# Performance work log

Hardware: AMD Instinct MI355X
Metric: run time of the kernel (lower is better)

The kernel has to match this reference:

```python
import jax, jax.numpy as jnp
import numpy as np

B, L, H, W, C = 8, 512, 768, 12, 25
S = L * W          # span_idx count, reshaped to [B, L, W, H]
Hh = H // 2        # per-direction LSTM hidden (bidirectional)


def setup_inputs() -> dict:
    key = jax.random.key(0)
    ks = jax.random.split(key, 24)
    p = lambda k, shape: jax.random.normal(k, shape, jnp.float32) * 0.02
    z = lambda n: jnp.zeros((n,), jnp.float32)
    return {
        "we": jax.random.normal(ks[0], (B, L, H), jnp.float32),
        "mask": jnp.ones((B, L), jnp.int32),
        "span_idx": jax.random.randint(ks[1], (B, S, 2), 0, L, jnp.int32),
        "pe": jax.random.normal(ks[2], (B, C, H), jnp.float32),
        # BiLSTM params (PyTorch gate order i,f,g,o)
        "w_ih_f": p(ks[3], (4 * Hh, H)), "w_hh_f": p(ks[4], (4 * Hh, Hh)),
        "b_ih_f": z(4 * Hh), "b_hh_f": z(4 * Hh),
        "w_ih_b": p(ks[5], (4 * Hh, H)), "w_hh_b": p(ks[6], (4 * Hh, Hh)),
        "b_ih_b": z(4 * Hh), "b_hh_b": z(4 * Hh),
        # project_start MLP: H -> 4H -> H
        "start_w1": p(ks[7], (4 * H, H)), "start_b1": z(4 * H),
        "start_w2": p(ks[8], (H, 4 * H)), "start_b2": z(H),
        # project_end MLP
        "end_w1": p(ks[9], (4 * H, H)), "end_b1": z(4 * H),
        "end_w2": p(ks[10], (H, 4 * H)), "end_b2": z(H),
        # out_project MLP: 2H -> 4H -> H
        "out_w1": p(ks[11], (4 * H, 2 * H)), "out_b1": z(4 * H),
        "out_w2": p(ks[12], (H, 4 * H)), "out_b2": z(H),
        # prompt_proj MLP: H -> 4H -> H
        "pr_w1": p(ks[13], (4 * H, H)), "pr_b1": z(4 * H),
        "pr_w2": p(ks[14], (H, 4 * H)), "pr_b2": z(H),
    }


def lstm_dir(x, w_ih, w_hh, b_ih, b_hh, reverse):
    # x: [B,L,D] -> per-direction hidden sequence [B,L,Hh]
    xg = jnp.einsum('bld,gd->blg', x, w_ih) + b_ih  # precomputed input gates
    n = w_hh.shape[1]

    def step(carry, xg_t):
        h, c = carry
        g = xg_t + h @ w_hh.T + b_hh
        i, f, gg, o = jnp.split(g, 4, axis=-1)
        c = jax.nn.sigmoid(f) * c + jax.nn.sigmoid(i) * jnp.tanh(gg)
        h = jax.nn.sigmoid(o) * jnp.tanh(c)
        return (h, c), h

    init = (jnp.zeros((x.shape[0], n), x.dtype), jnp.zeros((x.shape[0], n), x.dtype))
    _, hs = jax.lax.scan(step, init, jnp.swapaxes(xg, 0, 1), reverse=reverse)
    return jnp.swapaxes(hs, 0, 1)


def mlp(x, w1, b1, w2, b2):
    # Linear -> ReLU -> (Dropout: identity in eval) -> Linear
    return jax.nn.relu(x @ w1.T + b1) @ w2.T + b2


def extract_elements(t, idx):
    # t: [B,L,D], idx: [B,S] -> [B,S,D]; indices clamped like torch
    idx = jnp.clip(idx, 0, t.shape[1] - 1)
    return jnp.take_along_axis(t, idx[..., None], axis=1)


def reference(we, mask, span_idx, pe,
              w_ih_f, w_hh_f, b_ih_f, b_hh_f,
              w_ih_b, w_hh_b, b_ih_b, b_hh_b,
              start_w1, start_b1, start_w2, start_b2,
              end_w1, end_b1, end_w2, end_b2,
              out_w1, out_b1, out_w2, out_b2,
              pr_w1, pr_b1, pr_w2, pr_b2):
    # 1) Bidirectional LSTM encoder (pad_packed zeros masked positions)
    hf = lstm_dir(we, w_ih_f, w_hh_f, b_ih_f, b_hh_f, reverse=False)
    hb = lstm_dir(we, w_ih_b, w_hh_b, b_ih_b, b_hh_b, reverse=True)
    h = jnp.concatenate([hf, hb], axis=-1) * mask[..., None].astype(we.dtype)
    # 2) SpanMarkerV0: dual MLP -> gather -> concat+relu -> out MLP
    start_rep = mlp(h, start_w1, start_b1, start_w2, start_b2)
    end_rep = mlp(h, end_w1, end_b1, end_w2, end_b2)
    ss = extract_elements(start_rep, span_idx[:, :, 0])
    es = extract_elements(end_rep, span_idx[:, :, 1])
    cat = jax.nn.relu(jnp.concatenate([ss, es], axis=-1))
    span = mlp(cat, out_w1, out_b1, out_w2, out_b2).reshape(B, L, W, H)
    # 3) Prompt projection
    prompt = mlp(pe, pr_w1, pr_b1, pr_w2, pr_b2)
    return (span, prompt)
```

## Files before the change

### kernel.cpp

```cpp
#include <hip/hip_runtime.h>
#include <hip/hip_bf16.h>
#include <stdint.h>

#define B_ 8
#define L_ 512
#define H_ 768
#define WW_ 12
#define C_ 25
#define S_ (L_*WW_)
#define HH 384
#define G4 1536

using bf16x8 = __attribute__((ext_vector_type(8))) short;
using f32x4  = __attribute__((ext_vector_type(4))) float;

static __device__ __forceinline__ unsigned short f2bf(float x){
  unsigned u = __float_as_uint(x);
  unsigned r = (u + 0x7FFFu + ((u >> 16) & 1u)) >> 16;
  return (unsigned short)r;
}
static __device__ __forceinline__ float bflo(unsigned u){ return __uint_as_float(u << 16); }
static __device__ __forceinline__ float bfhi(unsigned u){ return __uint_as_float(u & 0xFFFF0000u); }

static __device__ __forceinline__ float sigmoid_f(float x){
  x = fminf(15.f, fmaxf(-15.f, x));
  return 1.f / (1.f + __expf(-x));
}
static __device__ __forceinline__ float tanh_f(float x){
  x = fminf(15.f, fmaxf(-15.f, x));
  float e = __expf(-2.f * x);
  return (1.f - e) / (1.f + e);
}

static __device__ __forceinline__ void gl_lds16(const unsigned short* g, unsigned short* l){
  __builtin_amdgcn_global_load_lds(
      (const __attribute__((address_space(1))) unsigned int*)g,
      (__attribute__((address_space(3))) unsigned int*)l,
      16, 0, 0);
}

__global__ void k_cast_bf16(const float* __restrict__ s, unsigned short* __restrict__ d, long n4){
  long i = (long)blockIdx.x * blockDim.x + threadIdx.x;
  if (i >= n4) return;
  float4 v = reinterpret_cast<const float4*>(s)[i];
  ushort4 o;
  o.x = f2bf(v.x); o.y = f2bf(v.y); o.z = f2bf(v.z); o.w = f2bf(v.w);
  reinterpret_cast<ushort4*>(d)[i] = o;
}

__global__ void k_biascomb(const float* __restrict__ a, const float* __restrict__ b,
                           float* __restrict__ o, int n){
  int i = blockIdx.x * blockDim.x + threadIdx.x;
  if (i < n) o[i] = a[i] + b[i];
}

template<int ACT, int OUTBF>
__global__ __launch_bounds__(256) void k_gemm2(
    const unsigned short* __restrict__ A, const unsigned short* __restrict__ Bm,
    const float* __restrict__ bias, void* __restrict__ Cout,
    int M, int N, int K, int ldb)
{
  __shared__ unsigned short Al[128 * 64];
  __shared__ unsigned short Bl[128 * 64];

  const int tid  = threadIdx.x;
  const int lane = tid & 63;
  const int wave = tid >> 6;
  const int wr = wave >> 1, wc = wave & 1;
  const int l16 = lane & 15, lq = lane >> 4;
  const int m0 = blockIdx.y * 128;
  const int n0 = blockIdx.x * 128;

  const int r_ = tid >> 3;
  const int p_ = tid & 7;
  const int cS = ((p_ ^ (r_ & 7)) * 8);
  const unsigned short* Asrc[4];
  const unsigned short* Bsrc[4];
  #pragma unroll
  for (int i = 0; i < 4; i++){
    int ra = m0 + i * 32 + r_; ra = ra < M ? ra : (M - 1);
    Asrc[i] = A + (size_t)ra * K + cS;
    int rb = n0 + i * 32 + r_; rb = rb < N ? rb : (N - 1);
    Bsrc[i] = Bm + (size_t)rb * ldb + cS;
  }

  f32x4 acc[4][4];
  #pragma unroll
  for (int a = 0; a < 4; a++)
    #pragma unroll
    for (int b = 0; b < 4; b++)
      acc[a][b] = (f32x4)0.f;

  const int sw0 = ((0 * 4 + lq) ^ (l16 & 7)) * 16;
  const int sw1 = ((1 * 4 + lq) ^ (l16 & 7)) * 16;
  const int aBase = (wr * 64 + l16) * 128;
  const int bBase = (wc * 64 + l16) * 128;

  for (int k0 = 0; k0 < K; k0 += 64){
    #pragma unroll
    for (int i = 0; i < 4; i++)
      gl_lds16(Asrc[i] + k0, Al + i * 2048 + tid * 8);
    #pragma unroll
    for (int i = 0; i < 4; i++)
      gl_lds16(Bsrc[i] + k0, Bl + i * 2048 + tid * 8);
    __syncthreads();

    #pragma unroll
    for (int kk = 0; kk < 2; kk++){
      const int sw = kk ? sw1 : sw0;
      bf16x8 av[4], bv[4];
      #pragma unroll
      for (int mi = 0; mi < 4; mi++)
        av[mi] = *reinterpret_cast<const bf16x8*>((const char*)Al + aBase + mi * 2048 + sw);
      #pragma unroll
      for (int ni = 0; ni < 4; ni++)
        bv[ni] = *reinterpret_cast<const bf16x8*>((const char*)Bl + bBase + ni * 2048 + sw);
      #pragma unroll
      for (int mi = 0; mi < 4; mi++)
        #pragma unroll
        for (int ni = 0; ni < 4; ni++)
          acc[mi][ni] = __builtin_amdgcn_mfma_f32_16x16x32_bf16(av[mi], bv[ni], acc[mi][ni], 0, 0, 0);
    }
    __syncthreads();
  }

  #pragma unroll
  for (int mi = 0; mi < 4; mi++){
    #pragma unroll
    for (int r = 0; r < 4; r++){
      int row = m0 + wr * 64 + mi * 16 + lq * 4 + r;
      if (row >= M) continue;
      #pragma unroll
      for (int ni = 0; ni < 4; ni++){
        int col = n0 + wc * 64 + ni * 16 + l16;
        float v = acc[mi][ni][r] + bias[col];
        if (ACT) v = v > 0.f ? v : 0.f;
        if (OUTBF) ((unsigned short*)Cout)[(size_t)row * N + col] = f2bf(v);
        else       ((float*)Cout)[(size_t)row * N + col] = v;
      }
    }
  }
}

__global__ __launch_bounds__(256) void k_gout(
    const unsigned short* __restrict__ Ps, const unsigned short* __restrict__ Pe,
    const int* __restrict__ sidx, const float* __restrict__ b1,
    const unsigned short* __restrict__ Bw, const float* __restrict__ b2,
    float* __restrict__ out)
{
  __shared__ unsigned short Al[128 * 64];
  __shared__ unsigned short Bl[128 * 64];
  __shared__ int idx2[128][2];

  const int tid  = threadIdx.x;
  const int lane = tid & 63;
  const int wave = tid >> 6;
  const int wr = wave >> 1, wc = wave & 1;
  const int l16 = lane & 15, lq = lane >> 4;
  const int tm = blockIdx.y;
  const int b  = tm / 48;
  const int s0 = (tm % 48) * 128;
  const int n0 = blockIdx.x * 128;

  if (tid < 128){
    int s = s0 + tid;
    int i0 = sidx[((size_t)b * S_ + s) * 2 + 0];
    int i1 = sidx[((size_t)b * S_ + s) * 2 + 1];
    idx2[tid][0] = min(max(i0, 0), L_ - 1);
    idx2[tid][1] = min(max(i1, 0), L_ - 1);
  }
  __syncthreads();

  const int r_ = tid >> 3;
  const int p_ = tid & 7;
  const int cS = ((p_ ^ (r_ & 7)) * 8);
  const unsigned short* Bsrc[4];
  const unsigned short* As0[4];
  const unsigned short* As1[4];
  #pragma unroll
  for (int i = 0; i < 4; i++){
    Bsrc[i] = Bw + (size_t)(n0 + i * 32 + r_) * 3072 + cS;
    int rr = i * 32 + r_;
    As0[i] = Ps + (size_t)(b * L_ + idx2[rr][0]) * 3072 + cS;
    As1[i] = Pe + (size_t)(b * L_ + idx2[rr][1]) * 3072 + cS;
  }

  f32x4 acc[4][4];
  #pragma unroll
  for (int a = 0; a < 4; a++)
    #pragma unroll
    for (int c = 0; c < 4; c++)
      acc[a][c] = (f32x4)0.f;

  const int sw0 = ((0 * 4 + lq) ^ (l16 & 7)) * 16;
  const int sw1 = ((1 * 4 + lq) ^ (l16 & 7)) * 16;
  const int aBase = (wr * 64 + l16) * 128;
  const int bBase = (wc * 64 + l16) * 128;

  for (int k0 = 0; k0 < 3072; k0 += 64){
    #pragma unroll
    for (int i = 0; i < 4; i++)
      gl_lds16(Bsrc[i] + k0, Bl + i * 2048 + tid * 8);
    float4 bb0 = *reinterpret_cast<const float4*>(b1 + k0 + cS);
    float4 bb1 = *reinterpret_cast<const float4*>(b1 + k0 + cS + 4);
    #pragma unroll
    for (int i = 0; i < 4; i++){
      uint4 va = *reinterpret_cast<const uint4*>(As0[i] + k0);
      uint4 ve = *reinterpret_cast<const uint4*>(As1[i] + k0);
      float f[8];
      f[0] = bflo(va.x) + bflo(ve.x) + bb0.x; f[1] = bfhi(va.x) + bfhi(ve.x) + bb0.y;
      f[2] = bflo(va.y) + bflo(ve.y) + bb0.z; f[3] = bfhi(va.y) + bfhi(ve.y) + bb0.w;
      f[4] = bflo(va.z) + bflo(ve.z) + bb1.x; f[5] = bfhi(va.z) + bfhi(ve.z) + bb1.y;
      f[6] = bflo(va.w) + bflo(ve.w) + bb1.z; f[7] = bfhi(va.w) + bfhi(ve.w) + bb1.w;
      unsigned short e[8];
      #pragma unroll
      for (int j = 0; j < 8; j++){ float v = f[j] > 0.f ? f[j] : 0.f; e[j] = f2bf(v); }
      uint4 rr;
      rr.x = (unsigned)e[0] | ((unsigned)e[1] << 16);
      rr.y = (unsigned)e[2] | ((unsigned)e[3] << 16);
      rr.z = (unsigned)e[4] | ((unsigned)e[5] << 16);
      rr.w = (unsigned)e[6] | ((unsigned)e[7] << 16);
      *reinterpret_cast<uint4*>(Al + i * 2048 + tid * 8) = rr;
    }
    __syncthreads();

    #pragma unroll
    for (int kk = 0; kk < 2; kk++){
      const int sw = kk ? sw1 : sw0;
      bf16x8 av[4], bv[4];
      #pragma unroll
      for (int mi = 0; mi < 4; mi++)
        av[mi] = *reinterpret_cast<const bf16x8*>((const char*)Al + aBase + mi * 2048 + sw);
      #pragma unroll
      for (int ni = 0; ni < 4; ni++)
        bv[ni] = *reinterpret_cast<const bf16x8*>((const char*)Bl + bBase + ni * 2048 + sw);
      #pragma unroll
      for (int mi = 0; mi < 4; mi++)
        #pragma unroll
        for (int ni = 0; ni < 4; ni++)
          acc[mi][ni] = __builtin_amdgcn_mfma_f32_16x16x32_bf16(av[mi], bv[ni], acc[mi][ni], 0, 0, 0);
    }
    __syncthreads();
  }

  #pragma unroll
  for (int mi = 0; mi < 4; mi++){
    #pragma unroll
    for (int r = 0; r < 4; r++){
      size_t row = (size_t)tm * 128 + wr * 64 + mi * 16 + lq * 4 + r;
      #pragma unroll
      for (int ni = 0; ni < 4; ni++){
        int col = n0 + wc * 64 + ni * 16 + l16;
        out[row * 768 + col] = acc[mi][ni][r] + b2[col];
      }
    }
  }
}

static __device__ __forceinline__ unsigned long long ald8(const unsigned long long* p){
  return __hip_atomic_load(p, __ATOMIC_RELAXED, __HIP_MEMORY_SCOPE_AGENT);
}

__global__ __launch_bounds__(512, 2) void k_lstm7(
    const float* __restrict__ xgf, const float* __restrict__ xgb,
    const unsigned short* __restrict__ Wbf,
    const int* __restrict__ mask,
    unsigned short* __restrict__ hbf,
    unsigned int* __restrict__ hg)
{
  const int dir  = blockIdx.x / 6;
  const int part = blockIdx.x % 6;
  const int tid  = threadIdx.x;
  const int lane = tid & 63;
  const int w    = tid >> 6;
  const int l16  = lane & 15, lq = lane >> 4;

  __shared__ alignas(16) unsigned short hls[8 * HH];
  __shared__ float gsl[256 * 9];

  const float* xg = dir ? xgb : xgf;
  const unsigned short* Wg = Wbf + (size_t)dir * G4 * HH;
  unsigned int* hgd = hg + dir * 2 * (8 * HH);

  bf16x8 bfr0[12], bfr1[12];
  {
    int r0 = w * 32 + l16;
    int r1 = w * 32 + 16 + l16;
    int g0 = r0 >> 6, j0u = r0 & 63;
    int g1 = r1 >> 6, j1u = r1 & 63;
    const unsigned short* p0 = Wg + ((size_t)g0 * HH + part * 64 + j0u) * HH + lq * 8;
    const unsigned short* p1 = Wg + ((size_t)g1 * HH + part * 64 + j1u) * HH + lq * 8;
    #pragma unroll
    for (int kf = 0; kf < 12; kf++){
      bfr0[kf] = *reinterpret_cast<const bf16x8*>(p0 + kf * 32);
      bfr1[kf] = *reinterpret_cast<const bf16x8*>(p1 + kf * 32);
    }
  }

  if (tid < 384) reinterpret_cast<uint4*>(hls)[tid] = uint4{0,0,0,0};

  const int cb = tid >> 6;
  const int cj = tid & 63;
  const int cu = part * 64 + cj;
  float c_state = 0.f;

  const int w0  = tid * 6;
  const int rb  = w0 / HH;
  const int ru  = w0 % HH;

  float xi, xf, xgg, xo, mvf;
  {
    const int t0 = dir ? (L_ - 1) : 0;
    const float* xr = xg + ((size_t)cb * L_ + t0) * G4;
    xi = xr[cu]; xf = xr[HH + cu]; xgg = xr[2 * HH + cu]; xo = xr[3 * HH + cu];
    mvf = (float)mask[cb * L_ + t0];
  }

  __syncthreads();

  for (int s = 0; s < L_; s++){
    const int t = dir ? (L_ - 1 - s) : s;

    float nxi = 0.f, nxf = 0.f, nxg = 0.f, nxo = 0.f, nmv = 0.f;
    if (s + 1 < L_){
      const int tn = dir ? (L_ - 2 - s) : (s + 1);
      const float* xr = xg + ((size_t)cb * L_ + tn) * G4;
      nxi = xr[cu]; nxf = xr[HH + cu]; nxg = xr[2 * HH + cu]; nxo = xr[3 * HH + cu];
      nmv = (float)mask[cb * L_ + tn];
    }

    if (s > 0){
      const unsigned long long tg = (unsigned long long)s;
      const unsigned long long* P =
        reinterpret_cast<const unsigned long long*>(hgd + ((s - 1) & 1) * (8 * HH) + w0);
      unsigned long long v0 = ald8(P), v1 = ald8(P + 1), v2 = ald8(P + 2);
      for (;;){
        bool ok0 = (((v0 >> 16) & 0xFFFFull) == tg) & ((v0 >> 48) == tg);
        bool ok1 = (((v1 >> 16) & 0xFFFFull) == tg) & ((v1 >> 48) == tg);
        bool ok2 = (((v2 >> 16) & 0xFFFFull) == tg) & ((v2 >> 48) == tg);
        if (ok0 & ok1 & ok2) break;
        v0 = ald8(P); v1 = ald8(P + 1); v2 = ald8(P + 2);
      }
      unsigned p01 = (unsigned)(v0 & 0xFFFFu) | ((unsigned)((v0 >> 32) & 0xFFFFu) << 16);
      unsigned p23 = (unsigned)(v1 & 0xFFFFu) | ((unsigned)((v1 >> 32) & 0xFFFFu) << 16);
      unsigned p45 = (unsigned)(v2 & 0xFFFFu) | ((unsigned)((v2 >> 32) & 0xFFFFu) << 16);
      *reinterpret_cast<unsigned*>((char*)hls + ((rb * 768 + (ru    ) * 2) ^ (rb << 4))) = p01;
      *reinterpret_cast<unsigned*>((char*)hls + ((rb * 768 + (ru + 2) * 2) ^ (rb << 4))) = p23;
      *reinterpret_cast<unsigned*>((char*)hls + ((rb * 768 + (ru + 4) * 2) ^ (rb << 4))) = p45;
    }
    __syncthreads();

    f32x4 acc0 = (f32x4)0.f, acc1 = (f32x4)0.f;
    const int arow = l16 & 7;
    #pragma unroll
    for (int kf = 0; kf < 12; kf++){
      int by = (arow * 768 + kf * 64 + lq * 16) ^ (arow << 4);
      bf16x8 a = *reinterpret_cast<const bf16x8*>((const char*)hls + by);
      acc0 = __builtin_amdgcn_mfma_f32_16x16x32_bf16(a, bfr0[kf], acc0, 0, 0, 0);
      acc1 = __builtin_amdgcn_mfma_f32_16x16x32_bf16(a, bfr1[kf], acc1, 0, 0, 0);
    }
    if (lq < 2){
      int n0r = w * 32 + l16;
      int n1r = w * 32 + 16 + l16;
      #pragma unroll
      for (int r = 0; r < 4; r++){
        gsl[n0r * 9 + lq * 4 + r] = acc0[r];
        gsl[n1r * 9 + lq * 4 + r] = acc1[r];
      }
    }
    __syncthreads();

    {
      float gi = gsl[(0 * 64 + cj) * 9 + cb] + xi;
      float gf = gsl[(1 * 64 + cj) * 9 + cb] + xf;
      float gg = gsl[(2 * 64 + cj) * 9 + cb] + xgg;
      float go = gsl[(3 * 64 + cj) * 9 + cb] + xo;
      c_state = sigmoid_f(gf) * c_state + sigmoid_f(gi) * tanh_f(gg);
      float h = sigmoid_f(go) * tanh_f(c_state);
      unsigned short hb = f2bf(h);
      *reinterpret_cast<unsigned short*>((char*)hls + ((cb * 768 + cu * 2) ^ (cb << 4))) = hb;
      unsigned word = ((unsigned)(s + 1) << 16) | (unsigned)hb;
      __hip_atomic_store(&hgd[(s & 1) * (8 * HH) + cb * HH + cu], word,
                         __ATOMIC_RELAXED, __HIP_MEMORY_SCOPE_AGENT);
      hbf[((size_t)cb * L_ + t) * H_ + dir * HH + cu] = f2bf(h * mvf);
    }

    xi = nxi; xf = nxf; xgg = nxg; xo = nxo; mvf = nmv;
  }
}

extern "C" void kernel_launch(void* const* d_in, const int* in_sizes, int n_in,
                              void* d_out, int out_size, void* d_ws, size_t ws_size,
                              hipStream_t stream)
{
  (void)in_sizes; (void)n_in; (void)out_size; (void)ws_size;
  const float* we     = (const float*)d_in[0];
  const int*   mask   = (const int*)  d_in[1];
  const int*   sidx   = (const int*)  d_in[2];
  const float* pe     = (const float*)d_in[3];
  const float* w_ih_f = (const float*)d_in[4];
  const float* w_hh_f = (const float*)d_in[5];
  const float* b_ih_f = (const float*)d_in[6];
  const float* b_hh_f = (const float*)d_in[7];
  const float* w_ih_b = (const float*)d_in[8];
  const float* w_hh_b = (const float*)d_in[9];
  const float* b_ih_b = (const float*)d_in[10];
  const float* b_hh_b = (const float*)d_in[11];
  const float* sw1 = (const float*)d_in[12]; const float* sb1 = (const float*)d_in[13];
  const float* sw2 = (const float*)d_in[14]; const float* sb2 = (const float*)d_in[15];
  const float* ew1 = (const float*)d_in[16]; const float* eb1 = (const float*)d_in[17];
  const float* ew2 = (const float*)d_in[18]; const float* eb2 = (const float*)d_in[19];
  const float* ow1 = (const float*)d_in[20]; const float* ob1 = (const float*)d_in[21];
  const float* ow2 = (const float*)d_in[22]; const float* ob2 = (const float*)d_in[23];
  const float* pw1 = (const float*)d_in[24]; const float* pb1 = (const float*)d_in[25];
  const float* pw2 = (const float*)d_in[26]; const float* pb2 = (const float*)d_in[27];

  char* wsp = (char*)d_ws; size_t off = 0;
  auto alloc = [&](size_t bytes) -> void* {
    void* p = wsp + off;
    off += (bytes + 255) & ~(size_t)255;
    return p;
  };

  unsigned short* we_bf   = (unsigned short*)alloc((size_t)4096*768*2);
  unsigned short* wihf_bf = (unsigned short*)alloc((size_t)1536*768*2);
  unsigned short* wihb_bf = (unsigned short*)alloc((size_t)1536*768*2);
  float* bc_f = (float*)alloc((size_t)1536*4);
  float* bc_b = (float*)alloc((size_t)1536*4);
  float* zerob = (float*)alloc((size_t)3072*4);
  float* xg_f = (float*)alloc((size_t)4096*1536*4);
  float* xg_b = (float*)alloc((size_t)4096*1536*4);
  unsigned short* whh_bf = (unsigned short*)alloc((size_t)2*1536*384*2);
  unsigned int* hg = (unsigned int*)alloc((size_t)2*2*8*384*4);
  unsigned short* h_bf  = (unsigned short*)alloc((size_t)4096*768*2);
  unsigned short* sw1b  = (unsigned short*)alloc((size_t)3072*768*2);
  unsigned short* sw2b  = (unsigned short*)alloc((size_t)768*3072*2);
  unsigned short* ew1b  = (unsigned short*)alloc((size_t)3072*768*2);
  unsigned short* ew2b  = (unsigned short*)alloc((size_t)768*3072*2);
  unsigned short* ow1b  = (unsigned short*)alloc((size_t)3072*1536*2);
  unsigned short* ow2b  = (unsigned short*)alloc((size_t)768*3072*2);
  unsigned short* pw1b  = (unsigned short*)alloc((size_t)3072*768*2);
  unsigned short* pw2b  = (unsigned short*)alloc((size_t)768*3072*2);
  unsigned short* srep  = (unsigned short*)alloc((size_t)4096*768*2);
  unsigned short* erep  = (unsigned short*)alloc((size_t)4096*768*2);
  unsigned short* midb  = (unsigned short*)alloc((size_t)4096*3072*2);
  unsigned short* pe_bf = (unsigned short*)alloc((size_t)200*768*2);
  unsigned short* pmid  = (unsigned short*)alloc((size_t)200*3072*2);

  unsigned short* Ps = (unsigned short*)xg_f;
  unsigned short* Pe = (unsigned short*)xg_b;

  auto cast = [&](const float* s, unsigned short* d, size_t n){
    long n4 = (long)(n / 4);
    int grid = (int)((n4 + 255) / 256);
    k_cast_bf16<<<grid, 256, 0, stream>>>(s, d, n4);
  };

  hipMemsetAsync(hg, 0, (size_t)2*2*8*384*4, stream);
  hipMemsetAsync(zerob, 0, (size_t)3072*4, stream);

  cast(we, we_bf, (size_t)4096*768);
  cast(w_ih_f, wihf_bf, (size_t)1536*768);
  cast(w_ih_b, wihb_bf, (size_t)1536*768);
  cast(w_hh_f, whh_bf,               (size_t)1536*384);
  cast(w_hh_b, whh_bf + 1536*384,    (size_t)1536*384);
  cast(sw1, sw1b, (size_t)3072*768);  cast(sw2, sw2b, (size_t)768*3072);
  cast(ew1, ew1b, (size_t)3072*768);  cast(ew2, ew2b, (size_t)768*3072);
  cast(ow1, ow1b, (size_t)3072*1536); cast(ow2, ow2b, (size_t)768*3072);
  cast(pw1, pw1b, (size_t)3072*768);  cast(pw2, pw2b, (size_t)768*3072);
  cast(pe, pe_bf, (size_t)200*768);

  k_biascomb<<<6, 256, 0, stream>>>(b_ih_f, b_hh_f, bc_f, 1536);
  k_biascomb<<<6, 256, 0, stream>>>(b_ih_b, b_hh_b, bc_b, 1536);

  dim3 blk(256);
  k_gemm2<0,0><<<dim3(12, 32), blk, 0, stream>>>(we_bf, wihf_bf, bc_f, xg_f, 4096, 1536, 768, 768);
  k_gemm2<0,0><<<dim3(12, 32), blk, 0, stream>>>(we_bf, wihb_bf, bc_b, xg_b, 4096, 1536, 768, 768);

  k_lstm7<<<12, 512, 0, stream>>>(xg_f, xg_b, whh_bf, mask, h_bf, hg);

  k_gemm2<1,1><<<dim3(24, 32), blk, 0, stream>>>(h_bf, sw1b, sb1, midb, 4096, 3072, 768, 768);
  k_gemm2<1,1><<<dim3( 6, 32), blk, 0, stream>>>(midb, sw2b, sb2, srep, 4096,  768, 3072, 3072);
  k_gemm2<1,1><<<dim3(24, 32), blk, 0, stream>>>(h_bf, ew1b, eb1, midb, 4096, 3072, 768, 768);
  k_gemm2<1,1><<<dim3( 6, 32), blk, 0, stream>>>(midb, ew2b, eb2, erep, 4096,  768, 3072, 3072);

  k_gemm2<0,1><<<dim3(24, 32), blk, 0, stream>>>(srep, ow1b,       zerob, Ps, 4096, 3072, 768, 1536);
  k_gemm2<0,1><<<dim3(24, 32), blk, 0, stream>>>(erep, ow1b + 768, zerob, Pe, 4096, 3072, 768, 1536);

  float* outp = (float*)d_out;
  k_gout<<<dim3(6, 384), blk, 0, stream>>>(Ps, Pe, sidx, ob1, ow2b, ob2, outp);

  k_gemm2<1,1><<<dim3(24, 2), blk, 0, stream>>>(pe_bf, pw1b, pb1, pmid, 200, 3072, 768, 768);
  k_gemm2<0,0><<<dim3( 6, 2), blk, 0, stream>>>(pmid, pw2b, pb2,
                                                outp + (size_t)37748736, 200, 768, 3072, 3072);
}
```

Baseline: 1.862 ms.

## Batch LSTM input-gate and start/end MLP GEMMs, prefetch gathered A in k_gout

Concatenates the forward and backward LSTM input-projection weights so a single GEMM writes a 3072-wide gate buffer, and the LSTM kernel reads it with a doubled row stride. Likewise, the start and end first-layer MLP weights are concatenated into one 6144-wide GEMM, and the two second-layer GEMMs read their halves through a new lda parameter. In the gather/output kernel, the gathered A rows and bias for the next k-step are loaded into registers ahead of the barrier so global latency overlaps the MFMA work. This cuts launch count and improves grid fill. In exchange the intermediate buffer doubles in size and register pressure rises in k_gout.

```diff
diff --git a/kernel.cpp b/kernel.cpp
--- a/kernel.cpp
+++ b/kernel.cpp
@@ -58,7 +58,7 @@
 __global__ __launch_bounds__(256) void k_gemm2(
     const unsigned short* __restrict__ A, const unsigned short* __restrict__ Bm,
     const float* __restrict__ bias, void* __restrict__ Cout,
-    int M, int N, int K, int ldb)
+    int M, int N, int K, int lda, int ldb)
 {
   __shared__ unsigned short Al[128 * 64];
   __shared__ unsigned short Bl[128 * 64];
@@ -79,7 +79,7 @@
   #pragma unroll
   for (int i = 0; i < 4; i++){
     int ra = m0 + i * 32 + r_; ra = ra < M ? ra : (M - 1);
-    Asrc[i] = A + (size_t)ra * K + cS;
+    Asrc[i] = A + (size_t)ra * lda + cS;
     int rb = n0 + i * 32 + r_; rb = rb < N ? rb : (N - 1);
     Bsrc[i] = Bm + (size_t)rb * ldb + cS;
   }
@@ -197,21 +197,30 @@
   const int aBase = (wr * 64 + l16) * 128;
   const int bBase = (wc * 64 + l16) * 128;
 
+  uint4 vaR[4], veR[4];
+  float4 bbR0, bbR1;
+  #pragma unroll
+  for (int i = 0; i < 4; i++){
+    vaR[i] = *reinterpret_cast<const uint4*>(As0[i]);
+    veR[i] = *reinterpret_cast<const uint4*>(As1[i]);
+  }
+  bbR0 = *reinterpret_cast<const float4*>(b1 + cS);
+  bbR1 = *reinterpret_cast<const float4*>(b1 + cS + 4);
+
   for (int k0 = 0; k0 < 3072; k0 += 64){
     #pragma unroll
     for (int i = 0; i < 4; i++)
       gl_lds16(Bsrc[i] + k0, Bl + i * 2048 + tid * 8);
-    float4 bb0 = *reinterpret_cast<const float4*>(b1 + k0 + cS);
-    float4 bb1 = *reinterpret_cast<const float4*>(b1 + k0 + cS + 4);
+
     #pragma unroll
     for (int i = 0; i < 4; i++){
-      uint4 va = *reinterpret_cast<const uint4*>(As0[i] + k0);
-      uint4 ve = *reinterpret_cast<const uint4*>(As1[i] + k0);
+      uint4 va = vaR[i];
+      uint4 ve = veR[i];
       float f[8];
-      f[0] = bflo(va.x) + bflo(ve.x) + bb0.x; f[1] = bfhi(va.x) + bfhi(ve.x) + bb0.y;
-      f[2] = bflo(va.y) + bflo(ve.y) + bb0.z; f[3] = bfhi(va.y) + bfhi(ve.y) + bb0.w;
-      f[4] = bflo(va.z) + bflo(ve.z) + bb1.x; f[5] = bfhi(va.z) + bfhi(ve.z) + bb1.y;
-      f[6] = bflo(va.w) + bflo(ve.w) + bb1.z; f[7] = bfhi(va.w) + bfhi(ve.w) + bb1.w;
+      f[0] = bflo(va.x) + bflo(ve.x) + bbR0.x; f[1] = bfhi(va.x) + bfhi(ve.x) + bbR0.y;
+      f[2] = bflo(va.y) + bflo(ve.y) + bbR0.z; f[3] = bfhi(va.y) + bfhi(ve.y) + bbR0.w;
+      f[4] = bflo(va.z) + bflo(ve.z) + bbR1.x; f[5] = bfhi(va.z) + bfhi(ve.z) + bbR1.y;
+      f[6] = bflo(va.w) + bflo(ve.w) + bbR1.z; f[7] = bfhi(va.w) + bfhi(ve.w) + bbR1.w;
       unsigned short e[8];
       #pragma unroll
       for (int j = 0; j < 8; j++){ float v = f[j] > 0.f ? f[j] : 0.f; e[j] = f2bf(v); }
@@ -222,6 +231,16 @@
       rr.w = (unsigned)e[6] | ((unsigned)e[7] << 16);
       *reinterpret_cast<uint4*>(Al + i * 2048 + tid * 8) = rr;
     }
+
+    if (k0 + 64 < 3072){
+      #pragma unroll
+      for (int i = 0; i < 4; i++){
+        vaR[i] = *reinterpret_cast<const uint4*>(As0[i] + k0 + 64);
+        veR[i] = *reinterpret_cast<const uint4*>(As1[i] + k0 + 64);
+      }
+      bbR0 = *reinterpret_cast<const float4*>(b1 + k0 + 64 + cS);
+      bbR1 = *reinterpret_cast<const float4*>(b1 + k0 + 64 + cS + 4);
+    }
     __syncthreads();
 
     #pragma unroll
@@ -262,7 +281,7 @@
 }
 
 __global__ __launch_bounds__(512, 2) void k_lstm7(
-    const float* __restrict__ xgf, const float* __restrict__ xgb,
+    const float* __restrict__ xgc,
     const unsigned short* __restrict__ Wbf,
     const int* __restrict__ mask,
     unsigned short* __restrict__ hbf,
@@ -278,7 +297,7 @@
   __shared__ alignas(16) unsigned short hls[8 * HH];
   __shared__ float gsl[256 * 9];
 
-  const float* xg = dir ? xgb : xgf;
+  const float* xg = xgc + dir * 1536;
   const unsigned short* Wg = Wbf + (size_t)dir * G4 * HH;
   unsigned int* hgd = hg + dir * 2 * (8 * HH);
 
@@ -311,7 +330,7 @@
   float xi, xf, xgg, xo, mvf;
   {
     const int t0 = dir ? (L_ - 1) : 0;
-    const float* xr = xg + ((size_t)cb * L_ + t0) * G4;
+    const float* xr = xg + ((size_t)cb * L_ + t0) * 3072;
     xi = xr[cu]; xf = xr[HH + cu]; xgg = xr[2 * HH + cu]; xo = xr[3 * HH + cu];
     mvf = (float)mask[cb * L_ + t0];
   }
@@ -324,7 +343,7 @@
     float nxi = 0.f, nxf = 0.f, nxg = 0.f, nxo = 0.f, nmv = 0.f;
     if (s + 1 < L_){
       const int tn = dir ? (L_ - 2 - s) : (s + 1);
-      const float* xr = xg + ((size_t)cb * L_ + tn) * G4;
+      const float* xr = xg + ((size_t)cb * L_ + tn) * 3072;
       nxi = xr[cu]; nxf = xr[HH + cu]; nxg = xr[2 * HH + cu]; nxo = xr[3 * HH + cu];
       nmv = (float)mask[cb * L_ + tn];
     }
@@ -422,20 +441,17 @@
     return p;
   };
 
-  unsigned short* we_bf   = (unsigned short*)alloc((size_t)4096*768*2);
-  unsigned short* wihf_bf = (unsigned short*)alloc((size_t)1536*768*2);
-  unsigned short* wihb_bf = (unsigned short*)alloc((size_t)1536*768*2);
-  float* bc_f = (float*)alloc((size_t)1536*4);
-  float* bc_b = (float*)alloc((size_t)1536*4);
+  unsigned short* we_bf  = (unsigned short*)alloc((size_t)4096*768*2);
+  unsigned short* wihc_bf= (unsigned short*)alloc((size_t)3072*768*2);
+  float* bcc   = (float*)alloc((size_t)3072*4);
   float* zerob = (float*)alloc((size_t)3072*4);
-  float* xg_f = (float*)alloc((size_t)4096*1536*4);
-  float* xg_b = (float*)alloc((size_t)4096*1536*4);
+  float* sbe1  = (float*)alloc((size_t)6144*4);
+  float* xgc   = (float*)alloc((size_t)4096*3072*4);
   unsigned short* whh_bf = (unsigned short*)alloc((size_t)2*1536*384*2);
   unsigned int* hg = (unsigned int*)alloc((size_t)2*2*8*384*4);
   unsigned short* h_bf  = (unsigned short*)alloc((size_t)4096*768*2);
-  unsigned short* sw1b  = (unsigned short*)alloc((size_t)3072*768*2);
+  unsigned short* swe1b = (unsigned short*)alloc((size_t)6144*768*2);
   unsigned short* sw2b  = (unsigned short*)alloc((size_t)768*3072*2);
-  unsigned short* ew1b  = (unsigned short*)alloc((size_t)3072*768*2);
   unsigned short* ew2b  = (unsigned short*)alloc((size_t)768*3072*2);
   unsigned short* ow1b  = (unsigned short*)alloc((size_t)3072*1536*2);
   unsigned short* ow2b  = (unsigned short*)alloc((size_t)768*3072*2);
@@ -443,12 +459,12 @@
   unsigned short* pw2b  = (unsigned short*)alloc((size_t)768*3072*2);
   unsigned short* srep  = (unsigned short*)alloc((size_t)4096*768*2);
   unsigned short* erep  = (unsigned short*)alloc((size_t)4096*768*2);
-  unsigned short* midb  = (unsigned short*)alloc((size_t)4096*3072*2);
+  unsigned short* midc  = (unsigned short*)alloc((size_t)4096*6144*2);
   unsigned short* pe_bf = (unsigned short*)alloc((size_t)200*768*2);
   unsigned short* pmid  = (unsigned short*)alloc((size_t)200*3072*2);
 
-  unsigned short* Ps = (unsigned short*)xg_f;
-  unsigned short* Pe = (unsigned short*)xg_b;
+  unsigned short* Ps = (unsigned short*)xgc;
+  unsigned short* Pe = (unsigned short*)xgc + (size_t)4096*3072;
 
   auto cast = [&](const float* s, unsigned short* d, size_t n){
     long n4 = (long)(n / 4);
@@ -458,39 +474,41 @@
 
   hipMemsetAsync(hg, 0, (size_t)2*2*8*384*4, stream);
   hipMemsetAsync(zerob, 0, (size_t)3072*4, stream);
+  hipMemcpyAsync(sbe1,        sb1, (size_t)3072*4, hipMemcpyDeviceToDevice, stream);
+  hipMemcpyAsync(sbe1 + 3072, eb1, (size_t)3072*4, hipMemcpyDeviceToDevice, stream);
 
   cast(we, we_bf, (size_t)4096*768);
-  cast(w_ih_f, wihf_bf, (size_t)1536*768);
-  cast(w_ih_b, wihb_bf, (size_t)1536*768);
+  cast(w_ih_f, wihc_bf,             (size_t)1536*768);
+  cast(w_ih_b, wihc_bf + 1536*768,  (size_t)1536*768);
   cast(w_hh_f, whh_bf,               (size_t)1536*384);
   cast(w_hh_b, whh_bf + 1536*384,    (size_t)1536*384);
-  cast(sw1, sw1b, (size_t)3072*768);  cast(sw2, sw2b, (size_t)768*3072);
-  cast(ew1, ew1b, (size_t)3072*768);  cast(ew2, ew2b, (size_t)768*3072);
+  cast(sw1, swe1b,             (size_t)3072*768);
+  cast(ew1, swe1b + 3072*768,  (size_t)3072*768);
+  cast(sw2, sw2b, (size_t)768*3072);
+  cast(ew2, ew2b, (size_t)768*3072);
   cast(ow1, ow1b, (size_t)3072*1536); cast(ow2, ow2b, (size_t)768*3072);
   cast(pw1, pw1b, (size_t)3072*768);  cast(pw2, pw2b, (size_t)768*3072);
   cast(pe, pe_bf, (size_t)200*768);
 
-  k_biascomb<<<6, 256, 0, stream>>>(b_ih_f, b_hh_f, bc_f, 1536);
-  k_biascomb<<<6, 256, 0, stream>>>(b_ih_b, b_hh_b, bc_b, 1536);
+  k_biascomb<<<6, 256, 0, stream>>>(b_ih_f, b_hh_f, bcc, 1536);
+  k_biascomb<<<6, 256, 0, stream>>>(b_ih_b, b_hh_b, bcc + 1536, 1536);
 
   dim3 blk(256);
-  k_gemm2<0,0><<<dim3(12, 32), blk, 0, stream>>>(we_bf, wihf_bf, bc_f, xg_f, 4096, 1536, 768, 768);
-  k_gemm2<0,0><<<dim3(12, 32), blk, 0, stream>>>(we_bf, wihb_bf, bc_b, xg_b, 4096, 1536, 768, 768);
-
-  k_lstm7<<<12, 512, 0, stream>>>(xg_f, xg_b, whh_bf, mask, h_bf, hg);
-
-  k_gemm2<1,1><<<dim3(24, 32), blk, 0, stream>>>(h_bf, sw1b, sb1, midb, 4096, 3072, 768, 768);
-  k_gemm2<1,1><<<dim3( 6, 32), blk, 0, stream>>>(midb, sw2b, sb2, srep, 4096,  768, 3072, 3072);
-  k_gemm2<1,1><<<dim3(24, 32), blk, 0, stream>>>(h_bf, ew1b, eb1, midb, 4096, 3072, 768, 768);
-  k_gemm2<1,1><<<dim3( 6, 32), blk, 0, stream>>>(midb, ew2b, eb2, erep, 4096,  768, 3072, 3072);
-
-  k_gemm2<0,1><<<dim3(24, 32), blk, 0, stream>>>(srep, ow1b,       zerob, Ps, 4096, 3072, 768, 1536);
-  k_gemm2<0,1><<<dim3(24, 32), blk, 0, stream>>>(erep, ow1b + 768, zerob, Pe, 4096, 3072, 768, 1536);
+  k_gemm2<0,0><<<dim3(24, 32), blk, 0, stream>>>(we_bf, wihc_bf, bcc, xgc, 4096, 3072, 768, 768, 768);
+
+  k_lstm7<<<12, 512, 0, stream>>>(xgc, whh_bf, mask, h_bf, hg);
+
+  k_gemm2<1,1><<<dim3(48, 32), blk, 0, stream>>>(h_bf, swe1b, sbe1, midc, 4096, 6144, 768, 768, 768);
+  k_gemm2<1,1><<<dim3(6, 32), blk, 0, stream>>>(midc,        sw2b, sb2, srep, 4096, 768, 3072, 6144, 3072);
+  k_gemm2<1,1><<<dim3(6, 32), blk, 0, stream>>>(midc + 3072, ew2b, eb2, erep, 4096, 768, 3072, 6144, 3072);
+
+  k_gemm2<0,1><<<dim3(24, 32), blk, 0, stream>>>(srep, ow1b,       zerob, Ps, 4096, 3072, 768, 768, 1536);
+  k_gemm2<0,1><<<dim3(24, 32), blk, 0, stream>>>(erep, ow1b + 768, zerob, Pe, 4096, 3072, 768, 768, 1536);
 
   float* outp = (float*)d_out;
   k_gout<<<dim3(6, 384), blk, 0, stream>>>(Ps, Pe, sidx, ob1, ow2b, ob2, outp);
 
-  k_gemm2<1,1><<<dim3(24, 2), blk, 0, stream>>>(pe_bf, pw1b, pb1, pmid, 200, 3072, 768, 768);
+  k_gemm2<1,1><<<dim3(24, 2), blk, 0, stream>>>(pe_bf, pw1b, pb1, pmid, 200, 3072, 768, 768, 768);
   k_gemm2<0,0><<<dim3( 6, 2), blk, 0, stream>>>(pmid, pw2b, pb2,
-                                                outp + (size_t)37748736, 200, 768, 3072, 3072);
-}
+                                                outp + (size_t)37748736, 200, 768, 3072, 3072, 3072);
+}
```

New measurement: 1.860 ms. No clear change (-0.1%).
